# Performance work log

Measured on AMD Instinct MI355X. Metric: run time of the kernel, lower is better.

The kernel has to match this reference:

```python
import jax, jax.numpy as jnp
import numpy as np

B, C, T, H, W, L = 4, 256, 8, 16, 16, 8
NO = 8                # num_offsets
D = C // NO           # per-head feature dim for offset/weight MLPs
EPS = 1e-5


def setup_inputs() -> dict:
    key = jax.random.key(0)
    ks = jax.random.split(key, 6)
    return {
        "features": jax.random.normal(ks[0], (B, C, T, H, W, L), jnp.float32),
        "pos": jax.random.normal(ks[1], (B, C, T, H, W, L), jnp.float32),
        "Wp": jax.random.normal(ks[2], (C, 3 * C), jnp.float32) * 0.02,  # 1x1x1 conv: 3C -> C
        "bp": jnp.zeros((C,), jnp.float32),
        "Wo": jax.random.normal(ks[3], (D, 3), jnp.float32) * 0.02,      # offset_embed Linear(d,3)
        "bo": jnp.zeros((3,), jnp.float32),
        "Ww": jax.random.normal(ks[4], (D, 2), jnp.float32) * 0.02,      # weight_embed Linear(d,2)
        "bw": jnp.zeros((2,), jnp.float32),
    }


def _trilinear_sample(feat, coords):
    """feat: (N,C,D1,D2,D3); coords: (N,G,3) in [-1,1] (axis order D1,D2,D3).
    align_corners=False, zeros padding (matches F.grid_sample semantics)."""
    N, Cc, D1, D2, D3 = feat.shape
    sizes = jnp.asarray([D1, D2, D3], feat.dtype)
    pix = ((coords + 1.0) * sizes - 1.0) * 0.5       # unnormalize to pixel coords
    lo = jnp.floor(pix)
    frac = pix - lo                                   # (N,G,3)
    lo = lo.astype(jnp.int32)
    dims = jnp.asarray([D1, D2, D3], jnp.int32)
    feat_flat = feat.reshape(N, Cc, D1 * D2 * D3)
    out = jnp.zeros((N, Cc, coords.shape[1]), feat.dtype)
    for dz in (0, 1):
        for dy in (0, 1):
            for dx in (0, 1):
                off = jnp.asarray([dz, dy, dx], jnp.int32)
                idx = lo + off                        # (N,G,3)
                wz = jnp.where(dz, frac[..., 0], 1.0 - frac[..., 0])
                wy = jnp.where(dy, frac[..., 1], 1.0 - frac[..., 1])
                wx = jnp.where(dx, frac[..., 2], 1.0 - frac[..., 2])
                wgt = wz * wy * wx                    # (N,G)
                valid = jnp.all((idx >= 0) & (idx < dims), axis=-1)
                idc = jnp.clip(idx, 0, dims - 1)
                lin = (idc[..., 0] * D2 + idc[..., 1]) * D3 + idc[..., 2]  # (N,G)
                vals = jnp.take_along_axis(feat_flat, lin[:, None, :], axis=2)  # (N,C,G)
                out = out + vals * (wgt * valid)[:, None, :]
    return out


def reference(features, pos, Wp, bp, Wo, bo, Ww, bw):
    Bv, Cv, Tv, Hv, Wv, Lv = features.shape
    BT = Bv * Tv
    feat = features.transpose(0, 2, 1, 3, 4, 5).reshape(BT, Cv, Hv, Wv, Lv)
    posr = pos.transpose(0, 2, 1, 3, 4, 5).reshape(BT, Cv, Hv, Wv, Lv)
    # global context + projection (1x1x1 conv over 3C channels) + ReLU
    glob = feat.mean(axis=(2, 3, 4), keepdims=True)
    src = jnp.concatenate([feat, posr, jnp.broadcast_to(glob, feat.shape)], axis=1)  # (BT,3C,H,W,L)
    proj = jax.nn.relu(jnp.einsum('nixyz,oi->noxyz', src, Wp) + bp[None, :, None, None, None])
    osrc = proj.transpose(0, 2, 3, 4, 1).reshape(BT, Hv, Wv, Lv, NO, D)
    # per-voxel per-head offsets in (0,1) and scalar weights
    offset = jax.nn.sigmoid(osrc @ Wo + bo)                      # (BT,H,W,L,NO,3)
    wgt = jax.nn.softmax(osrc @ Ww + bw, axis=-1)[..., 1]        # (BT,H,W,L,NO)
    # base flow field in [-1,1], deform in logit space, re-sigmoid
    base = jnp.stack(jnp.meshgrid(jnp.linspace(-1.0, 1.0, Hv),
                                  jnp.linspace(-1.0, 1.0, Wv),
                                  jnp.linspace(-1.0, 1.0, Lv), indexing='ij'), axis=-1)
    base01 = jnp.clip((base + 1.0) * 0.5, EPS, 1.0 - EPS)
    logit = jnp.log(base01 / (1.0 - base01))                     # (H,W,L,3)
    sp = jax.nn.sigmoid(logit[None, :, :, :, None, :] + offset)  # (BT,H,W,L,NO,3)
    grid = (sp * 2.0 - 1.0).transpose(0, 4, 1, 2, 3, 5).reshape(BT, NO * Hv * Wv * Lv, 3)
    sampled = _trilinear_sample(feat, grid).reshape(BT, Cv, NO, Hv, Wv, Lv)
    out = feat + jnp.einsum('bcnhwl,bhwln->bchwl', sampled, wgt)
    return out.reshape(Bv, Tv, Cv, Hv, Wv, Lv).transpose(0, 2, 1, 3, 4, 5)
```

## Files before the change

### kernel.cpp

```cpp
#include <hip/hip_runtime.h>

#define BB 4
#define CC 256
#define TT 8
#define HH 16
#define WW 16
#define LL 8
#define NO 8
#define DD 32
#define BT 32
#define VV 2048
#define KIN 512
#define EPS_ 1e-5f

typedef short bf16x8 __attribute__((ext_vector_type(8)));
typedef float f32x4 __attribute__((ext_vector_type(4)));
typedef float f32x2 __attribute__((ext_vector_type(2)));

static __device__ __forceinline__ float b2f(unsigned short u) {
    return __uint_as_float(((unsigned int)u) << 16);
}
static __device__ __forceinline__ float b2f_lo(unsigned int x) {
    return __uint_as_float(x << 16);
}
static __device__ __forceinline__ float b2f_hi(unsigned int x) {
    return __uint_as_float(x & 0xffff0000u);
}
static __device__ __forceinline__ unsigned short f2b(float f) {
    unsigned int x = __float_as_uint(f);
    unsigned int r = x + 0x7fffu + ((x >> 16) & 1u);
    return (unsigned short)(r >> 16);
}
static __device__ __forceinline__ unsigned int f2b_pk(float lo, float hi) {
    return (unsigned int)f2b(lo) | ((unsigned int)f2b(hi) << 16);
}
static __device__ __forceinline__ float sigm(float x) {
    return 1.0f / (1.0f + __expf(-x));
}

__global__ __launch_bounds__(256) void k0_prep(const float* __restrict__ Wp,
                                               unsigned short* __restrict__ Wa) {
    int i = blockIdx.x * 256 + threadIdx.x;
    int o = i >> 9, k = i & 511;
    Wa[i] = f2b(Wp[o * 768 + k]);
}

__global__ __launch_bounds__(256) void k1_transpose(const float* __restrict__ features,
                                                    const float* __restrict__ pos,
                                                    unsigned short* __restrict__ srcT,
                                                    float* __restrict__ gpart) {
    const int n = blockIdx.x;
    const int vt = blockIdx.y;
    const int v0 = vt * 16;
    const int b = n >> 3, t = n & 7;
    const int tid = threadIdx.x;
    const int ty = tid >> 4;
    const int tx = tid & 15;

    __shared__ unsigned short s1[16 * 520];

    for (int cb = 0; cb < CC; cb += 16) {
        int c = cb + ty;
        size_t fidx = (((size_t)b * CC + c) * TT + t) * VV + v0 + tx;
        float f = features[fidx];
        float p = pos[fidx];
        s1[tx * 520 + c] = f2b(f);
        s1[tx * 520 + 256 + c] = f2b(p);
        for (int d = 8; d > 0; d >>= 1) f += __shfl_down(f, d, 16);
        if (tx == 0) gpart[((size_t)n * 128 + vt) * CC + c] = f;
    }
    __syncthreads();
    const size_t base = ((size_t)n * VV + v0) * KIN;
    for (int q = tid; q < 1024; q += 256) {
        int row = q >> 6;
        int koff = (q & 63) * 8;
        *(uint4*)&srcT[base + (size_t)row * KIN + koff] = *(const uint4*)&s1[row * 520 + koff];
    }
}

__global__ __launch_bounds__(256) void k2_gterm(const float* __restrict__ gpart,
                                                const float* __restrict__ Wp,
                                                const float* __restrict__ bp,
                                                float* __restrict__ gterm) {
    const int n = blockIdx.x;
    const int o = threadIdx.x;
    __shared__ float gl[CC];
    float s = 0.0f;
    const float* gp = gpart + (size_t)n * 128 * CC + o;
    #pragma unroll 8
    for (int vt = 0; vt < 128; ++vt) s += gp[(size_t)vt * CC];
    gl[o] = s * (1.0f / (float)VV);
    __syncthreads();
    const float4* wrow = (const float4*)(Wp + (size_t)o * 768 + 512);
    const float4* g4 = (const float4*)gl;
    float acc = bp[o];
    #pragma unroll 8
    for (int c = 0; c < 64; ++c) {
        float4 w = wrow[c], g = g4[c];
        acc += w.x * g.x + w.y * g.y + w.z * g.z + w.w * g.w;
    }
    gterm[n * CC + o] = acc;
}

__global__ __launch_bounds__(256) void k3_gemm(const unsigned short* __restrict__ Wa,
                                               const unsigned short* __restrict__ srcT,
                                               const float* __restrict__ gterm,
                                               unsigned short* __restrict__ projT) {
    const int n  = blockIdx.x;
    const int mb = blockIdx.y;
    const int nb = blockIdx.z;
    const int tid = threadIdx.x;
    const int m0 = mb * 128, v0 = nb * 128;

    __shared__ short As[128 * 40];
    __shared__ short Bs[128 * 40];

    const int wv = tid >> 6;
    const int lane = tid & 63;
    const int wm = wv >> 1, wn = wv & 1;
    const int lr = lane & 15, lq = lane >> 4;

    f32x4 acc[4][4];
    #pragma unroll
    for (int i = 0; i < 4; ++i)
        #pragma unroll
        for (int j = 0; j < 4; ++j)
            acc[i][j] = (f32x4){0.f, 0.f, 0.f, 0.f};

    const int row = tid >> 1, half = tid & 1;
    const unsigned short* agp = Wa + (size_t)(m0 + row) * KIN + half * 16;
    const unsigned short* bgp = srcT + ((size_t)n * VV + v0 + row) * KIN + half * 16;
    short* asp = &As[row * 40 + half * 16];
    short* bsp = &Bs[row * 40 + half * 16];

    for (int k0 = 0; k0 < KIN; k0 += 32) {
        uint4 a0 = *(const uint4*)(agp + k0);
        uint4 a1 = *(const uint4*)(agp + k0 + 8);
        uint4 b0 = *(const uint4*)(bgp + k0);
        uint4 b1 = *(const uint4*)(bgp + k0 + 8);
        __syncthreads();
        *(uint4*)asp = a0; *(uint4*)(asp + 8) = a1;
        *(uint4*)bsp = b0; *(uint4*)(bsp + 8) = b1;
        __syncthreads();

        bf16x8 af[4], bf[4];
        #pragma unroll
        for (int i = 0; i < 4; ++i)
            af[i] = *(const bf16x8*)&As[(wm * 64 + i * 16 + lr) * 40 + lq * 8];
        #pragma unroll
        for (int j = 0; j < 4; ++j)
            bf[j] = *(const bf16x8*)&Bs[(wn * 64 + j * 16 + lr) * 40 + lq * 8];
        #pragma unroll
        for (int i = 0; i < 4; ++i)
            #pragma unroll
            for (int j = 0; j < 4; ++j)
                acc[i][j] = __builtin_amdgcn_mfma_f32_16x16x32_bf16(af[i], bf[j], acc[i][j], 0, 0, 0);
    }

    #pragma unroll
    for (int i = 0; i < 4; ++i) {
        const int og = m0 + wm * 64 + i * 16 + lq * 4;
        float4 g = *(const float4*)(gterm + n * CC + og);
        #pragma unroll
        for (int j = 0; j < 4; ++j) {
            const int vg = v0 + wn * 64 + j * 16 + lr;
            float x0 = fmaxf(acc[i][j][0] + g.x, 0.0f);
            float x1 = fmaxf(acc[i][j][1] + g.y, 0.0f);
            float x2 = fmaxf(acc[i][j][2] + g.z, 0.0f);
            float x3 = fmaxf(acc[i][j][3] + g.w, 0.0f);
            ushort4 st;
            st.x = f2b(x0); st.y = f2b(x1); st.z = f2b(x2); st.w = f2b(x3);
            *(ushort4*)&projT[((size_t)n * VV + vg) * CC + og] = st;
        }
    }
}

__global__ __launch_bounds__(256) void k4_coef(const unsigned short* __restrict__ projT,
                                               const float* __restrict__ Wo,
                                               const float* __restrict__ bo,
                                               const float* __restrict__ Ww,
                                               const float* __restrict__ bw,
                                               int2* __restrict__ pairs) {
    __shared__ float sWo[96], sWw[64], sb[5];
    const int tid = threadIdx.x;
    if (tid < 96) sWo[tid] = Wo[tid];
    if (tid < 64) sWw[tid] = Ww[tid];
    if (tid < 3)  sb[tid] = bo[tid];
    if (tid < 2)  sb[3 + tid] = bw[tid];
    __syncthreads();

    const int g = blockIdx.x * 256 + tid;
    const int n = g >> 14;
    const int rem = g & 16383;
    const int v = rem >> 3;
    const int hd = rem & 7;

    const uint4* up = (const uint4*)(projT + ((size_t)n * VV + v) * CC + hd * DD);
    float osrc[32];
    #pragma unroll
    for (int q = 0; q < 4; ++q) {
        uint4 u = up[q];
        unsigned int ws4[4] = {u.x, u.y, u.z, u.w};
        #pragma unroll
        for (int e = 0; e < 4; ++e) {
            osrc[q * 8 + e * 2]     = b2f_lo(ws4[e]);
            osrc[q * 8 + e * 2 + 1] = b2f_hi(ws4[e]);
        }
    }

    float o0 = sb[0], o1 = sb[1], o2 = sb[2];
    float zw = sb[4] - sb[3];
    #pragma unroll
    for (int d = 0; d < DD; ++d) {
        float t = osrc[d];
        o0 += t * sWo[3 * d + 0];
        o1 += t * sWo[3 * d + 1];
        o2 += t * sWo[3 * d + 2];
        zw += t * (sWw[2 * d + 1] - sWw[2 * d]);
    }
    const float wgt = sigm(zw);

    const int h = v >> 7, w = (v >> 3) & 15, l = v & 7;
    float ph = fminf(fmaxf(h * (1.0f / 15.0f), EPS_), 1.0f - EPS_);
    float pw = fminf(fmaxf(w * (1.0f / 15.0f), EPS_), 1.0f - EPS_);
    float pl = fminf(fmaxf(l * (1.0f / 7.0f),  EPS_), 1.0f - EPS_);
    float lh = __logf(ph / (1.0f - ph));
    float lw = __logf(pw / (1.0f - pw));
    float ll = __logf(pl / (1.0f - pl));

    float sph = sigm(lh + sigm(o0));
    float spw = sigm(lw + sigm(o1));
    float spl = sigm(ll + sigm(o2));
    float pixh = sph * 16.0f - 0.5f;
    float pixw = spw * 16.0f - 0.5f;
    float pixl = spl * 8.0f  - 0.5f;

    float flh = floorf(pixh), flw = floorf(pixw), fll = floorf(pixl);
    float fh = pixh - flh, fw = pixw - flw, fl = pixl - fll;
    int ih = (int)flh, iw = (int)flw, il = (int)fll;

    int2* pp = pairs + (size_t)g * 8;
    #pragma unroll
    for (int dz = 0; dz < 2; ++dz)
        #pragma unroll
        for (int dy = 0; dy < 2; ++dy)
            #pragma unroll
            for (int dx = 0; dx < 2; ++dx) {
                int iz = ih + dz, iy = iw + dy, ix = il + dx;
                float wt = (dz ? fh : 1.0f - fh) * (dy ? fw : 1.0f - fw) * (dx ? fl : 1.0f - fl) * wgt;
                bool valid = ((unsigned)iz < 16u) && ((unsigned)iy < 16u) && ((unsigned)ix < 8u);
                int lin = valid ? (((iz * 16 + iy) * 8 + ix) << 10) : 0;
                float wv2 = valid ? wt : 0.0f;
                pp[dz * 4 + dy * 2 + dx] = make_int2(lin, __float_as_int(wv2));
            }
}

__global__ __launch_bounds__(256) void k5_gather(const unsigned short* __restrict__ srcT,
                                                 const int2* __restrict__ pairs,
                                                 unsigned short* __restrict__ res) {
    __shared__ int2 pr[8 * 64];
    const int n  = blockIdx.x >> 8;
    const int vb = (blockIdx.x & 255) * 8;
    const int tid = threadIdx.x;

    {
        const int2* src = pairs + ((size_t)n * VV + vb) * 64;
        *(int4*)&pr[tid * 2] = *(const int4*)&src[tid * 2];
    }
    __syncthreads();

    const int s = tid >> 5;
    const int lane = tid & 31;
    const unsigned int laneoff = (unsigned int)lane * 16u;
    const char* slabB = (const char*)srcT + (size_t)n * VV * KIN * 2;
    const int2* pe = &pr[s * 64];

    f32x2 a0 = {0.f, 0.f}, a1 = {0.f, 0.f}, a2 = {0.f, 0.f}, a3 = {0.f, 0.f};

    #pragma unroll 1
    for (int e = 0; e < 64; e += 8) {
        uint4 f[8];
        float w[8];
        #pragma unroll
        for (int u = 0; u < 8; ++u) {
            int2 q = pe[e + u];
            w[u] = __int_as_float(q.y);
            f[u] = *(const uint4*)(slabB + ((unsigned int)q.x + laneoff));
        }
        #pragma unroll
        for (int u = 0; u < 8; ++u) {
            f32x2 w2 = {w[u], w[u]};
            f32x2 t0 = {b2f_lo(f[u].x), b2f_hi(f[u].x)};
            f32x2 t1 = {b2f_lo(f[u].y), b2f_hi(f[u].y)};
            f32x2 t2 = {b2f_lo(f[u].z), b2f_hi(f[u].z)};
            f32x2 t3 = {b2f_lo(f[u].w), b2f_hi(f[u].w)};
            a0 = __builtin_elementwise_fma(w2, t0, a0);
            a1 = __builtin_elementwise_fma(w2, t1, a1);
            a2 = __builtin_elementwise_fma(w2, t2, a2);
            a3 = __builtin_elementwise_fma(w2, t3, a3);
        }
    }

    uint4 st;
    st.x = f2b_pk(a0.x, a0.y);
    st.y = f2b_pk(a1.x, a1.y);
    st.z = f2b_pk(a2.x, a2.y);
    st.w = f2b_pk(a3.x, a3.y);
    *(uint4*)&res[((size_t)n * VV + vb + s) * CC + lane * 8] = st;
}

__global__ __launch_bounds__(256) void k6_final(const float* __restrict__ features,
                                                const unsigned short* __restrict__ res,
                                                float* __restrict__ out) {
    const int n = blockIdx.x;
    const int c0 = blockIdx.y * 64;
    const int v0 = blockIdx.z * 64;
    const int b = n >> 3, t = n & 7;
    const int tid = threadIdx.x;
    const int ty = tid >> 6, tx = tid & 63;

    __shared__ unsigned short t6[64 * 66];

    for (int vv = ty; vv < 64; vv += 4)
        t6[vv * 66 + tx] = res[((size_t)n * VV + v0 + vv) * CC + c0 + tx];
    __syncthreads();
    for (int cc = ty; cc < 64; cc += 4) {
        int c = c0 + cc;
        size_t oidx = (((size_t)b * CC + c) * TT + t) * VV + v0 + tx;
        out[oidx] = features[oidx] + b2f(t6[tx * 66 + cc]);
    }
}

extern "C" void kernel_launch(void* const* d_in, const int* in_sizes, int n_in,
                              void* d_out, int out_size, void* d_ws, size_t ws_size,
                              hipStream_t stream) {
    (void)in_sizes; (void)n_in; (void)out_size; (void)ws_size;
    const float* features = (const float*)d_in[0];
    const float* pos      = (const float*)d_in[1];
    const float* Wp       = (const float*)d_in[2];
    const float* bp       = (const float*)d_in[3];
    const float* Wo       = (const float*)d_in[4];
    const float* bo       = (const float*)d_in[5];
    const float* Ww       = (const float*)d_in[6];
    const float* bw       = (const float*)d_in[7];
    float* out = (float*)d_out;

    char* ws = (char*)d_ws;
    unsigned short* srcT  = (unsigned short*)ws;
    unsigned short* Wa    = (unsigned short*)(ws + 67108864);
    float*          gterm = (float*)(ws + 67403776);
    unsigned short* projT = (unsigned short*)(ws + 67436544);
    int2*           pairs = (int2*)(ws + 100990976);
    float*          gpart = (float*)(ws + 100990976);
    unsigned short* res   = projT;

    k0_prep<<<512, 256, 0, stream>>>(Wp, Wa);
    k1_transpose<<<dim3(32, 128), 256, 0, stream>>>(features, pos, srcT, gpart);
    k2_gterm<<<32, 256, 0, stream>>>(gpart, Wp, bp, gterm);
    k3_gemm<<<dim3(32, 2, 16), 256, 0, stream>>>(Wa, srcT, gterm, projT);
    k4_coef<<<2048, 256, 0, stream>>>(projT, Wo, bo, Ww, bw, pairs);
    k5_gather<<<8192, 256, 0, stream>>>(srcT, pairs, res);
    k6_final<<<dim3(32, 4, 32), 256, 0, stream>>>(features, res, out);
}
```

Measured before the change: 373.3 us.

## Widen transpose tile and move global-mean reduction into separate kernel

The transpose kernel now handles 32 voxels per block with 128-byte coalesced reads per half-wave, uses separate padded shared buffers for features and pos, and writes 32-bit words. The per-channel spatial partial sums that were computed with shuffles inside the transpose move to a new kernel that re-reads the bf16 transposed source. The aim is to make the large transpose pass bandwidth-efficient at the cost of an extra launch and a second read of srcT, and the mean is now computed from bf16-rounded values instead of fp32.

```diff
diff --git a/kernel.cpp b/kernel.cpp
--- a/kernel.cpp
+++ b/kernel.cpp
@@ -47,35 +47,61 @@
 
 __global__ __launch_bounds__(256) void k1_transpose(const float* __restrict__ features,
                                                     const float* __restrict__ pos,
-                                                    unsigned short* __restrict__ srcT,
-                                                    float* __restrict__ gpart) {
+                                                    unsigned short* __restrict__ srcT) {
     const int n = blockIdx.x;
     const int vt = blockIdx.y;
-    const int v0 = vt * 16;
+    const int v0 = vt * 32;
     const int b = n >> 3, t = n & 7;
     const int tid = threadIdx.x;
-    const int ty = tid >> 4;
-    const int tx = tid & 15;
-
-    __shared__ unsigned short s1[16 * 520];
-
-    for (int cb = 0; cb < CC; cb += 16) {
-        int c = cb + ty;
-        size_t fidx = (((size_t)b * CC + c) * TT + t) * VV + v0 + tx;
-        float f = features[fidx];
-        float p = pos[fidx];
-        s1[tx * 520 + c] = f2b(f);
-        s1[tx * 520 + 256 + c] = f2b(p);
-        for (int d = 8; d > 0; d >>= 1) f += __shfl_down(f, d, 16);
-        if (tx == 0) gpart[((size_t)n * 128 + vt) * CC + c] = f;
-    }
-    __syncthreads();
-    const size_t base = ((size_t)n * VV + v0) * KIN;
-    for (int q = tid; q < 1024; q += 256) {
-        int row = q >> 6;
-        int koff = (q & 63) * 8;
-        *(uint4*)&srcT[base + (size_t)row * KIN + koff] = *(const uint4*)&s1[row * 520 + koff];
-    }
+    const int wv = tid >> 6;
+    const int half = (tid >> 5) & 1;
+    const int vl = tid & 31;
+
+    __shared__ unsigned short sf[32 * 258];
+    __shared__ unsigned short sp[32 * 258];
+
+    const size_t base_ft = ((size_t)b * CC * TT + t) * (size_t)VV + v0 + vl;
+    #pragma unroll 8
+    for (int it = 0; it < 32; ++it) {
+        const int c = it * 8 + wv * 2 + half;
+        const size_t idx = base_ft + (size_t)c * (TT * VV);
+        float f = features[idx];
+        float p = pos[idx];
+        sf[vl * 258 + c] = f2b(f);
+        sp[vl * 258 + c] = f2b(p);
+    }
+    __syncthreads();
+
+    unsigned int* srcU = (unsigned int*)srcT;
+    const size_t obase = ((size_t)n * VV + v0) * 256;
+    const int ku = tid;
+    #pragma unroll 4
+    for (int v = 0; v < 32; ++v) {
+        unsigned int u;
+        if (ku < 128) u = *(const unsigned int*)&sf[v * 258 + 2 * ku];
+        else          u = *(const unsigned int*)&sp[v * 258 + 2 * (ku - 128)];
+        srcU[obase + (size_t)v * 256 + ku] = u;
+    }
+}
+
+__global__ __launch_bounds__(256) void k2a_gsum(const unsigned short* __restrict__ srcT,
+                                                float* __restrict__ gpart) {
+    const int n = blockIdx.x;
+    const int vs = blockIdx.y;
+    const int tid = threadIdx.x;
+    const int ku = tid & 127;
+    const int vh = tid >> 7;
+    const unsigned int* srcU = (const unsigned int*)srcT;
+    const size_t base = ((size_t)n * VV + vs * 128 + vh * 64) * 256 + ku;
+    float sl = 0.f, sh = 0.f;
+    #pragma unroll 8
+    for (int i = 0; i < 64; ++i) {
+        unsigned int u = srcU[base + (size_t)i * 256];
+        sl += b2f_lo(u);
+        sh += b2f_hi(u);
+    }
+    float2* gp = (float2*)gpart;
+    gp[((size_t)n * 32 + vs * 2 + vh) * 128 + ku] = make_float2(sl, sh);
 }
 
 __global__ __launch_bounds__(256) void k2_gterm(const float* __restrict__ gpart,
@@ -86,9 +112,9 @@
     const int o = threadIdx.x;
     __shared__ float gl[CC];
     float s = 0.0f;
-    const float* gp = gpart + (size_t)n * 128 * CC + o;
+    const float* gp = gpart + (size_t)n * 32 * CC + o;
     #pragma unroll 8
-    for (int vt = 0; vt < 128; ++vt) s += gp[(size_t)vt * CC];
+    for (int vt = 0; vt < 32; ++vt) s += gp[vt * CC];
     gl[o] = s * (1.0f / (float)VV);
     __syncthreads();
     const float4* wrow = (const float4*)(Wp + (size_t)o * 768 + 512);
@@ -355,7 +381,8 @@
     unsigned short* res   = projT;
 
     k0_prep<<<512, 256, 0, stream>>>(Wp, Wa);
-    k1_transpose<<<dim3(32, 128), 256, 0, stream>>>(features, pos, srcT, gpart);
+    k1_transpose<<<dim3(32, 64), 256, 0, stream>>>(features, pos, srcT);
+    k2a_gsum<<<dim3(32, 16), 256, 0, stream>>>(srcT, gpart);
     k2_gterm<<<32, 256, 0, stream>>>(gpart, Wp, bp, gterm);
     k3_gemm<<<dim3(32, 2, 16), 256, 0, stream>>>(Wa, srcT, gterm, projT);
     k4_coef<<<2048, 256, 0, stream>>>(projT, Wo, bo, Ww, bw, pairs);
```

Result: no change. 371.5 us (-0.5%).
